# Performance work log

Hardware: AMD Instinct MI355X
Metric: run time of the kernel (lower is better)

Reference implementation:

```python
import jax, jax.numpy as jnp
import numpy as np

NUM_ACTIVE = 2  # top-k active experts

def setup_inputs() -> dict:
    key = jax.random.key(0)
    ks = jax.random.split(key, 5)
    B, N, D, H, E = 8192, 16, 128, 384, 8
    x = jax.random.normal(ks[0], (B, N, D), dtype=jnp.float32)
    # xavier-ish scales for stability
    router_w = jax.random.normal(ks[1], (E, N * D), dtype=jnp.float32) * (1.0 / np.sqrt(N * D))
    w1 = jax.random.normal(ks[2], (E, N, D, H), dtype=jnp.float32) * (1.0 / np.sqrt(D))
    w_gate = jax.random.normal(ks[3], (E, N, D, H), dtype=jnp.float32) * (1.0 / np.sqrt(D))
    w2 = jax.random.normal(ks[4], (E, N, H, D), dtype=jnp.float32) * (1.0 / np.sqrt(H))
    return {"x": x, "router_w": router_w, "w1": w1, "w_gate": w_gate, "w2": w2}

def reference(x, router_w, w1, w_gate, w2):
    B, N, D = x.shape
    E = w1.shape[0]
    # shared router over flattened heads
    router_logits = x.reshape(B, N * D) @ router_w.T            # (B, E)
    topk_logits, topk_idx = jax.lax.top_k(router_logits, NUM_ACTIVE)
    topk_w = jax.nn.softmax(topk_logits, axis=-1)               # (B, K)
    # combined routing weight per (token, expert); zero if expert not selected
    onehot = jax.nn.one_hot(topk_idx, E, dtype=x.dtype)         # (B, K, E)
    w_tok_exp = jnp.einsum('bk,bke->be', topk_w, onehot)        # (B, E)
    out = jnp.zeros_like(x)
    # loop over fixed, small expert count; unselected tokens get weight 0
    for e in range(E):
        h1 = jnp.einsum('bnd,ndh->bnh', x, w1[e])
        gate = jnp.einsum('bnd,ndh->bnh', x, w_gate[e])
        h = h1 * jax.nn.silu(gate)                              # SwiGLU (dropout=0 / eval)
        out_e = jnp.einsum('bnh,nhd->bnd', h, w2[e])
        out = out + w_tok_exp[:, e][:, None, None] * out_e
    return out
```

## Files before the change

kernel.cpp:

```cpp
#include <hip/hip_runtime.h>

#define NTOK  8192
#define NHEAD 16
#define DDIM  128
#define HDIM  384
#define NEXP  8
#define TILE  128
#define ENTRIES 1280

typedef __attribute__((ext_vector_type(8))) short short8;
typedef __attribute__((ext_vector_type(4))) float f32x4;

#define SZ_WP    (128UL*12*24*512*2)
#define OFF_WP   0UL
#define OFF_ROUT (OFF_WP + SZ_WP)
#define OFF_CNT  (OFF_ROUT + 8192UL*16)
#define OFF_TAB  (OFF_CNT + 256)
#define OFF_LIST (OFF_TAB + 2UL*ENTRIES*16)
#define OFF_WL   (OFF_LIST + 2UL*8192*4)

struct Routing { int i0, i1; float w0, w1; };

__device__ __forceinline__ unsigned short f2bf(float f) {
  unsigned int u = __float_as_uint(f);
  u += 0x7fffu + ((u >> 16) & 1u);
  return (unsigned short)(u >> 16);
}

__device__ __forceinline__ void dma16(const unsigned short* g, char* l) {
  __builtin_amdgcn_global_load_lds(
      (const __attribute__((address_space(1))) unsigned int*)g,
      (__attribute__((address_space(3))) unsigned int*)l, 16, 0, 0);
}

__global__ __launch_bounds__(256) void convA_kernel(
    const float* __restrict__ w1, const float* __restrict__ wg,
    unsigned short* __restrict__ wP) {
  __shared__ float ls[32][388];
  const int kk = blockIdx.x;
  const int en = blockIdx.y;
  const int z  = blockIdx.z;
  const float* src = (z == 0 ? w1 : wg) + ((size_t)en * DDIM + kk * 32) * HDIM;
  const int tid = threadIdx.x;
  #pragma unroll
  for (int i = 0; i < 12; ++i) {
    int f4 = i * 256 + tid;
    int row = f4 / 96, c4 = f4 % 96;
    float4 v = reinterpret_cast<const float4*>(src + (size_t)row * HDIM)[c4];
    ls[row][c4*4+0] = v.x; ls[row][c4*4+1] = v.y;
    ls[row][c4*4+2] = v.z; ls[row][c4*4+3] = v.w;
  }
  __syncthreads();
  #pragma unroll
  for (int i = 0; i < 6; ++i) {
    int fid = i * 256 + tid;
    int ct = fid >> 6, lane = fid & 63;
    int r0 = (lane >> 4) * 8, c = ct * 16 + (lane & 15);
    unsigned short o[8];
    #pragma unroll
    for (int j = 0; j < 8; ++j) o[j] = f2bf(ls[r0 + j][c]);
    size_t off = (((size_t)en * 12 + (ct >> 1)) * 24 + (z * 8 + kk * 2 + (ct & 1))) * 512
               + (size_t)lane * 8;
    reinterpret_cast<uint4*>(wP + off)[0] =
        make_uint4((unsigned)o[0] | ((unsigned)o[1] << 16),
                   (unsigned)o[2] | ((unsigned)o[3] << 16),
                   (unsigned)o[4] | ((unsigned)o[5] << 16),
                   (unsigned)o[6] | ((unsigned)o[7] << 16));
  }
}

__global__ __launch_bounds__(256) void convB_kernel(
    const float* __restrict__ w2, unsigned short* __restrict__ wP) {
  __shared__ float ls[32][132];
  const int kk = blockIdx.x;
  const int en = blockIdx.y;
  const float* src = w2 + ((size_t)en * HDIM + kk * 32) * DDIM;
  const int tid = threadIdx.x;
  #pragma unroll
  for (int i = 0; i < 4; ++i) {
    int f4 = i * 256 + tid;
    int row = f4 >> 5, c4 = f4 & 31;
    float4 v = reinterpret_cast<const float4*>(src + (size_t)row * DDIM)[c4];
    ls[row][c4*4+0] = v.x; ls[row][c4*4+1] = v.y;
    ls[row][c4*4+2] = v.z; ls[row][c4*4+3] = v.w;
  }
  __syncthreads();
  #pragma unroll
  for (int i = 0; i < 2; ++i) {
    int fid = i * 256 + tid;
    int ct = fid >> 6, lane = fid & 63;
    int r0 = (lane >> 4) * 8, c = ct * 16 + (lane & 15);
    unsigned short o[8];
    #pragma unroll
    for (int j = 0; j < 8; ++j) o[j] = f2bf(ls[r0 + j][c]);
    size_t off = (((size_t)en * 12 + kk) * 24 + (16 + ct)) * 512 + (size_t)lane * 8;
    reinterpret_cast<uint4*>(wP + off)[0] =
        make_uint4((unsigned)o[0] | ((unsigned)o[1] << 16),
                   (unsigned)o[2] | ((unsigned)o[3] << 16),
                   (unsigned)o[4] | ((unsigned)o[5] << 16),
                   (unsigned)o[6] | ((unsigned)o[7] << 16));
  }
}

__global__ __launch_bounds__(256) void router_kernel(
    const float* __restrict__ x, const float* __restrict__ rw,
    Routing* __restrict__ routing) {
  const int lane = threadIdx.x & 63;
  const int wgid = blockIdx.x * 4 + (threadIdx.x >> 6);
  const int tok0 = wgid * 4;
  float acc[4][8];
  #pragma unroll
  for (int t = 0; t < 4; ++t)
    #pragma unroll
    for (int e = 0; e < 8; ++e) acc[t][e] = 0.f;
  const float4* xr = reinterpret_cast<const float4*>(x);
  const float4* wr = reinterpret_cast<const float4*>(rw);
  #pragma unroll
  for (int c = 0; c < 8; ++c) {
    float4 wv[8];
    #pragma unroll
    for (int e = 0; e < 8; ++e) wv[e] = wr[e * 512 + c * 64 + lane];
    #pragma unroll
    for (int t = 0; t < 4; ++t) {
      float4 xv = xr[(size_t)(tok0 + t) * 512 + c * 64 + lane];
      #pragma unroll
      for (int e = 0; e < 8; ++e)
        acc[t][e] += xv.x * wv[e].x + xv.y * wv[e].y + xv.z * wv[e].z + xv.w * wv[e].w;
    }
  }
  #pragma unroll
  for (int t = 0; t < 4; ++t)
    #pragma unroll
    for (int e = 0; e < 8; ++e) {
      acc[t][e] += __shfl_xor(acc[t][e], 1);
      acc[t][e] += __shfl_xor(acc[t][e], 2);
      acc[t][e] += __shfl_xor(acc[t][e], 4);
    }
  const int l3 = lane & 7;
  #pragma unroll
  for (int t = 0; t < 4; ++t) {
    float v0 = (l3 & 1) ? acc[t][1] : acc[t][0];
    float v1 = (l3 & 1) ? acc[t][3] : acc[t][2];
    float v2 = (l3 & 1) ? acc[t][5] : acc[t][4];
    float v3 = (l3 & 1) ? acc[t][7] : acc[t][6];
    float u0 = (l3 & 2) ? v1 : v0;
    float u1 = (l3 & 2) ? v3 : v2;
    float sel = (l3 & 4) ? u1 : u0;
    sel += __shfl_xor(sel, 8);
    sel += __shfl_xor(sel, 16);
    sel += __shfl_xor(sel, 32);
    float le[8];
    #pragma unroll
    for (int e = 0; e < 8; ++e) le[e] = __shfl(sel, e);
    if (lane == 0) {
      int tok = tok0 + t;
      int i0 = 0; float m0 = le[0];
      #pragma unroll
      for (int e = 1; e < 8; ++e) if (le[e] > m0) { m0 = le[e]; i0 = e; }
      int i1 = -1; float m1 = -3.4e38f;
      #pragma unroll
      for (int e = 0; e < 8; ++e) if (e != i0 && le[e] > m1) { m1 = le[e]; i1 = e; }
      float ed = __expf(m1 - m0);
      Routing r; r.i0 = i0; r.i1 = i1;
      r.w0 = 1.f / (1.f + ed); r.w1 = ed / (1.f + ed);
      routing[tok] = r;
    }
  }
}

__global__ __launch_bounds__(256) void count_kernel(
    const Routing* __restrict__ routing, int* __restrict__ cnt) {
  const int s = blockIdx.x >> 3, e = blockIdx.x & 7;
  const int tid = threadIdx.x;
  int c = 0;
  for (int t = tid; t < NTOK; t += 256) {
    Routing r = routing[t];
    c += ((s == 0 ? r.i0 : r.i1) == e);
  }
  c += __shfl_xor(c, 32); c += __shfl_xor(c, 16); c += __shfl_xor(c, 8);
  c += __shfl_xor(c, 4);  c += __shfl_xor(c, 2);  c += __shfl_xor(c, 1);
  __shared__ int wsum[4];
  if ((tid & 63) == 0) wsum[tid >> 6] = c;
  __syncthreads();
  if (tid == 0) cnt[blockIdx.x] = wsum[0] + wsum[1] + wsum[2] + wsum[3];
}

__global__ void build_kernel(const int* __restrict__ cnt, int* __restrict__ cur,
                             int4* __restrict__ table) {
  const int tid = threadIdx.x;
  for (int i = tid; i < 2 * ENTRIES; i += 256)
    table[i] = make_int4(0, 0, 0, 0);
  __syncthreads();
  if (tid < 16) {
    int s = tid >> 3, e = tid & 7;
    int base = 0;
    for (int k = 0; k < e; ++k) base += cnt[s * 8 + k];
    cur[tid] = base;
  }
  __syncthreads();
  if (tid < 16) {
    int s = tid >> 3, xcd = tid & 7;
    int j = 0;
    int base = 0;
    for (int e = 0; e < 8; ++e) {
      int c = cnt[s * 8 + e];
      #pragma unroll
      for (int nn = 0; nn < 2; ++nn) {
        int n = xcd + nn * 8;
        for (int t = 0; t < c; t += TILE) {
          int rc = c - t; if (rc > TILE) rc = TILE;
          table[s * ENTRIES + xcd + 8 * j] = make_int4(e, base + t, rc, n);
          ++j;
        }
      }
      base += c;
    }
  }
}

__global__ __launch_bounds__(256) void compact_kernel(
    const Routing* __restrict__ routing, const int* __restrict__ cur,
    int* __restrict__ list, float* __restrict__ wl) {
  const int s = blockIdx.x >> 3, e = blockIdx.x & 7;
  const int tid = threadIdx.x;
  __shared__ int ps[256];
  int myc = 0;
  for (int t = tid; t < NTOK; t += 256) {
    Routing r = routing[t];
    myc += ((s == 0 ? r.i0 : r.i1) == e);
  }
  ps[tid] = myc;
  __syncthreads();
  for (int off = 1; off < 256; off <<= 1) {
    int v = (tid >= off) ? ps[tid - off] : 0;
    __syncthreads();
    ps[tid] += v;
    __syncthreads();
  }
  int base = cur[blockIdx.x] + ps[tid] - myc;
  for (int t = tid; t < NTOK; t += 256) {
    Routing r = routing[t];
    int ei = (s == 0 ? r.i0 : r.i1);
    if (ei == e) {
      list[s * NTOK + base] = t;
      wl[s * NTOK + base] = (s == 0 ? r.w0 : r.w1);
      ++base;
    }
  }
}

__global__ __launch_bounds__(512, 4) void expert_kernel(
    const float* __restrict__ x,
    const unsigned short* __restrict__ wP,
    const int* __restrict__ list, const float* __restrict__ wl,
    const int4* __restrict__ table,
    float* __restrict__ out, const int slot)
{
  extern __shared__ char smem[];
  char* wb  = smem;
  char* pwb = smem + 49152;
  const int4 tb = table[slot * ENTRIES + blockIdx.x];
  const int e = tb.x, rbeg = tb.y, rcnt = tb.z, n = tb.w;
  if (rcnt == 0) return;
  const int* lst = list + slot * NTOK + rbeg;
  const float* wls = wl + slot * NTOK + rbeg;
  const int tid = threadIdx.x;
  const int wid = tid >> 6, lane = tid & 63;
  const int lr = lane & 15, lq = lane >> 4;
  const int tq = wid >> 1, ch = wid & 1;
  char* pq = pwb + tq * 2304;
  const f32x4 z4 = {0.f, 0.f, 0.f, 0.f};

  const unsigned short* wsrc = wP + (size_t)(e * NHEAD + n) * (12 * 24 * 512);

  short8 a[2][4];
  #pragma unroll
  for (int mi = 0; mi < 2; ++mi) {
    int row = tq * 32 + mi * 16 + lr;
    int ok = (row < rcnt);
    int tok = ok ? lst[row] : 0;
    const float* xp = x + ((size_t)tok * NHEAD + n) * DDIM;
    #pragma unroll
    for (int kk = 0; kk < 4; ++kk) {
      const float4* q = reinterpret_cast<const float4*>(xp + kk * 32 + lq * 8);
      float4 v0 = q[0], v1 = q[1];
      if (!ok) { v0 = make_float4(0,0,0,0); v1 = make_float4(0,0,0,0); }
      short8 t;
      t[0] = (short)f2bf(v0.x); t[1] = (short)f2bf(v0.y);
      t[2] = (short)f2bf(v0.z); t[3] = (short)f2bf(v0.w);
      t[4] = (short)f2bf(v1.x); t[5] = (short)f2bf(v1.y);
      t[6] = (short)f2bf(v1.z); t[7] = (short)f2bf(v1.w);
      a[mi][kk] = t;
    }
  }

  f32x4 acc[2][4];
  #pragma unroll
  for (int mi = 0; mi < 2; ++mi)
    #pragma unroll
    for (int ct = 0; ct < 4; ++ct) acc[mi][ct] = z4;

  #pragma unroll
  for (int i = 0; i < 3; ++i) {
    int seg = wid * 3 + i;
    dma16(wsrc + (size_t)seg * 512 + lane * 8, wb + seg * 1024);
  }

  #pragma unroll
  for (int c = 0; c < 12; ++c) {
    const int p = c & 1;
    char* wbp = wb + p * 24576;

    asm volatile("s_waitcnt lgkmcnt(0)" ::: "memory");
    __builtin_amdgcn_s_barrier();
    __builtin_amdgcn_sched_barrier(0);

    if (c < 11) {
      char* wbn = wb + (p ^ 1) * 24576;
      #pragma unroll
      for (int i = 0; i < 3; ++i) {
        int seg = wid * 3 + i;
        dma16(wsrc + ((size_t)(c + 1) * 24 + seg) * 512 + lane * 8, wbn + seg * 1024);
      }
      asm volatile("s_waitcnt vmcnt(3)" ::: "memory");
    } else {
      asm volatile("s_waitcnt vmcnt(0)" ::: "memory");
    }
    __builtin_amdgcn_s_barrier();
    __builtin_amdgcn_sched_barrier(0);

    {
      f32x4 ah[2], ag[2];
      ah[0] = ah[1] = z4; ag[0] = ag[1] = z4;
      #pragma unroll
      for (int kk = 0; kk < 4; ++kk) {
        short8 b1 = *reinterpret_cast<const short8*>(wbp + (kk * 2 + ch) * 1024 + lane * 16);
        short8 bg = *reinterpret_cast<const short8*>(wbp + 8192 + (kk * 2 + ch) * 1024 + lane * 16);
        #pragma unroll
        for (int mi = 0; mi < 2; ++mi) {
          ah[mi] = __builtin_amdgcn_mfma_f32_16x16x32_bf16(a[mi][kk], b1, ah[mi], 0, 0, 0);
          ag[mi] = __builtin_amdgcn_mfma_f32_16x16x32_bf16(a[mi][kk], bg, ag[mi], 0, 0, 0);
        }
      }
      #pragma unroll
      for (int mi = 0; mi < 2; ++mi)
        #pragma unroll
        for (int r = 0; r < 4; ++r) {
          float h1 = ah[mi][r], g = ag[mi][r];
          float val = h1 * g * __builtin_amdgcn_rcpf(1.f + __expf(-g));
          int rowq = mi * 16 + lq * 4 + r;
          int h = ch * 16 + lr;
          *reinterpret_cast<unsigned short*>(pq + rowq * 72 + h * 2) = f2bf(val);
        }
    }

    asm volatile("s_waitcnt lgkmcnt(0)" ::: "memory");
    __builtin_amdgcn_s_barrier();
    __builtin_amdgcn_sched_barrier(0);

    {
      short8 a2[2];
      #pragma unroll
      for (int mi = 0; mi < 2; ++mi)
        a2[mi] = *reinterpret_cast<const short8*>(pq + (mi * 16 + lr) * 72 + lq * 16);
      #pragma unroll
      for (int ct = 0; ct < 4; ++ct) {
        short8 b = *reinterpret_cast<const short8*>(wbp + (16 + ch * 4 + ct) * 1024 + lane * 16);
        acc[0][ct] = __builtin_amdgcn_mfma_f32_16x16x32_bf16(a2[0], b, acc[0][ct], 0, 0, 0);
        acc[1][ct] = __builtin_amdgcn_mfma_f32_16x16x32_bf16(a2[1], b, acc[1][ct], 0, 0, 0);
      }
    }
  }

  #pragma unroll
  for (int mi = 0; mi < 2; ++mi)
    #pragma unroll
    for (int r = 0; r < 4; ++r) {
      int row = tq * 32 + mi * 16 + lq * 4 + r;
      if (row < rcnt) {
        int tok = lst[row];
        float wt = wls[row];
        float* op = out + ((size_t)tok * NHEAD + n) * DDIM;
        #pragma unroll
        for (int ct = 0; ct < 4; ++ct) {
          int col = (ch * 4 + ct) * 16 + lr;
          float v = acc[mi][ct][r] * wt;
          if (slot == 0) op[col] = v;
          else          op[col] += v;
        }
      }
    }
}

extern "C" void kernel_launch(void* const* d_in, const int* in_sizes, int n_in,
                              void* d_out, int out_size, void* d_ws, size_t ws_size,
                              hipStream_t stream) {
  const float* x  = (const float*)d_in[0];
  const float* rw = (const float*)d_in[1];
  const float* w1 = (const float*)d_in[2];
  const float* wg = (const float*)d_in[3];
  const float* w2 = (const float*)d_in[4];
  float* out = (float*)d_out;
  char* ws = (char*)d_ws;

  unsigned short* wP = (unsigned short*)(ws + OFF_WP);
  Routing* routing = (Routing*)(ws + OFF_ROUT);
  int* cnt = (int*)(ws + OFF_CNT);
  int* cur = cnt + 16;
  int4* table = (int4*)(ws + OFF_TAB);
  int* list = (int*)(ws + OFF_LIST);
  float* wl = (float*)(ws + OFF_WL);

  convA_kernel<<<dim3(4, 128, 2), 256, 0, stream>>>(w1, wg, wP);
  convB_kernel<<<dim3(12, 128, 1), 256, 0, stream>>>(w2, wP);
  router_kernel<<<512, 256, 0, stream>>>(x, rw, routing);
  count_kernel<<<16, 256, 0, stream>>>(routing, cnt);
  build_kernel<<<1, 256, 0, stream>>>(cnt, cur, table);
  compact_kernel<<<16, 256, 0, stream>>>(routing, cur, list, wl);
  expert_kernel<<<ENTRIES, 512, 58368, stream>>>(
      x, wP, list, wl, table, out, 0);
  expert_kernel<<<ENTRIES, 512, 58368, stream>>>(
      x, wP, list, wl, table, out, 1);
}
```

Measured before the change: 274.0 us.

## Group tokens by expert pair and fuse both expert passes into one kernel

```diff
diff --git a/kernel.cpp b/kernel.cpp
--- a/kernel.cpp
+++ b/kernel.cpp
@@ -6,7 +6,8 @@
 #define HDIM  384
 #define NEXP  8
 #define TILE  128
-#define ENTRIES 1280
+#define NPAIR 64
+#define ENTRIES 2176
 
 typedef __attribute__((ext_vector_type(8))) short short8;
 typedef __attribute__((ext_vector_type(4))) float f32x4;
@@ -15,9 +16,10 @@
 #define OFF_WP   0UL
 #define OFF_ROUT (OFF_WP + SZ_WP)
 #define OFF_CNT  (OFF_ROUT + 8192UL*16)
-#define OFF_TAB  (OFF_CNT + 256)
-#define OFF_LIST (OFF_TAB + 2UL*ENTRIES*16)
-#define OFF_WL   (OFF_LIST + 2UL*8192*4)
+#define OFF_TAB  (OFF_CNT + 512)
+#define OFF_LIST (OFF_TAB + (size_t)ENTRIES*16)
+#define OFF_WL0  (OFF_LIST + 8192UL*4)
+#define OFF_WL1  (OFF_WL0 + 8192UL*4)
 
 struct Routing { int i0, i1; float w0, w1; };
 
@@ -170,46 +172,44 @@
 
 __global__ __launch_bounds__(256) void count_kernel(
     const Routing* __restrict__ routing, int* __restrict__ cnt) {
-  const int s = blockIdx.x >> 3, e = blockIdx.x & 7;
+  const int p = blockIdx.x;
   const int tid = threadIdx.x;
   int c = 0;
   for (int t = tid; t < NTOK; t += 256) {
     Routing r = routing[t];
-    c += ((s == 0 ? r.i0 : r.i1) == e);
+    c += ((r.i0 * 8 + r.i1) == p);
   }
   c += __shfl_xor(c, 32); c += __shfl_xor(c, 16); c += __shfl_xor(c, 8);
   c += __shfl_xor(c, 4);  c += __shfl_xor(c, 2);  c += __shfl_xor(c, 1);
   __shared__ int wsum[4];
   if ((tid & 63) == 0) wsum[tid >> 6] = c;
   __syncthreads();
-  if (tid == 0) cnt[blockIdx.x] = wsum[0] + wsum[1] + wsum[2] + wsum[3];
+  if (tid == 0) cnt[p] = wsum[0] + wsum[1] + wsum[2] + wsum[3];
 }
 
 __global__ void build_kernel(const int* __restrict__ cnt, int* __restrict__ cur,
                              int4* __restrict__ table) {
   const int tid = threadIdx.x;
-  for (int i = tid; i < 2 * ENTRIES; i += 256)
+  for (int i = tid; i < ENTRIES; i += 256)
     table[i] = make_int4(0, 0, 0, 0);
   __syncthreads();
-  if (tid < 16) {
-    int s = tid >> 3, e = tid & 7;
-    int base = 0;
-    for (int k = 0; k < e; ++k) base += cnt[s * 8 + k];
-    cur[tid] = base;
-  }
-  __syncthreads();
-  if (tid < 16) {
-    int s = tid >> 3, xcd = tid & 7;
-    int j = 0;
-    int base = 0;
-    for (int e = 0; e < 8; ++e) {
-      int c = cnt[s * 8 + e];
+  if (tid < NPAIR) {
+    int b = 0;
+    for (int k = 0; k < tid; ++k) b += cnt[k];
+    cur[tid] = b;
+  }
+  __syncthreads();
+  if (tid < 8) {
+    int xcd = tid;
+    int j = 0, base = 0;
+    for (int p = 0; p < NPAIR; ++p) {
+      int c = cnt[p];
       #pragma unroll
       for (int nn = 0; nn < 2; ++nn) {
         int n = xcd + nn * 8;
         for (int t = 0; t < c; t += TILE) {
           int rc = c - t; if (rc > TILE) rc = TILE;
-          table[s * ENTRIES + xcd + 8 * j] = make_int4(e, base + t, rc, n);
+          table[xcd + 8 * j] = make_int4(p, base + t, rc, n);
           ++j;
         }
       }
@@ -220,14 +220,14 @@
 
 __global__ __launch_bounds__(256) void compact_kernel(
     const Routing* __restrict__ routing, const int* __restrict__ cur,
-    int* __restrict__ list, float* __restrict__ wl) {
-  const int s = blockIdx.x >> 3, e = blockIdx.x & 7;
+    int* __restrict__ list, float* __restrict__ wl0, float* __restrict__ wl1) {
+  const int p = blockIdx.x;
   const int tid = threadIdx.x;
   __shared__ int ps[256];
   int myc = 0;
   for (int t = tid; t < NTOK; t += 256) {
     Routing r = routing[t];
-    myc += ((s == 0 ? r.i0 : r.i1) == e);
+    myc += ((r.i0 * 8 + r.i1) == p);
   }
   ps[tid] = myc;
   __syncthreads();
@@ -237,33 +237,36 @@
     ps[tid] += v;
     __syncthreads();
   }
-  int base = cur[blockIdx.x] + ps[tid] - myc;
+  int base = cur[p] + ps[tid] - myc;
   for (int t = tid; t < NTOK; t += 256) {
     Routing r = routing[t];
-    int ei = (s == 0 ? r.i0 : r.i1);
-    if (ei == e) {
-      list[s * NTOK + base] = t;
-      wl[s * NTOK + base] = (s == 0 ? r.w0 : r.w1);
+    if ((r.i0 * 8 + r.i1) == p) {
+      list[base] = t;
+      wl0[base] = r.w0;
+      wl1[base] = r.w1;
       ++base;
     }
   }
 }
 
-__global__ __launch_bounds__(512, 4) void expert_kernel(
+__global__ __launch_bounds__(512, 3) void expert_kernel(
     const float* __restrict__ x,
     const unsigned short* __restrict__ wP,
-    const int* __restrict__ list, const float* __restrict__ wl,
+    const int* __restrict__ list,
+    const float* __restrict__ wl0, const float* __restrict__ wl1,
     const int4* __restrict__ table,
-    float* __restrict__ out, const int slot)
+    float* __restrict__ out)
 {
   extern __shared__ char smem[];
   char* wb  = smem;
   char* pwb = smem + 49152;
-  const int4 tb = table[slot * ENTRIES + blockIdx.x];
-  const int e = tb.x, rbeg = tb.y, rcnt = tb.z, n = tb.w;
+  const int4 tb = table[blockIdx.x];
+  const int pair = tb.x, rbeg = tb.y, rcnt = tb.z, n = tb.w;
   if (rcnt == 0) return;
-  const int* lst = list + slot * NTOK + rbeg;
-  const float* wls = wl + slot * NTOK + rbeg;
+  const int e0 = pair >> 3, e1 = pair & 7;
+  const int* lst = list + rbeg;
+  const float* wls0 = wl0 + rbeg;
+  const float* wls1 = wl1 + rbeg;
   const int tid = threadIdx.x;
   const int wid = tid >> 6, lane = tid & 63;
   const int lr = lane & 15, lq = lane >> 4;
@@ -271,7 +274,8 @@
   char* pq = pwb + tq * 2304;
   const f32x4 z4 = {0.f, 0.f, 0.f, 0.f};
 
-  const unsigned short* wsrc = wP + (size_t)(e * NHEAD + n) * (12 * 24 * 512);
+  const unsigned short* wsrc0 = wP + (size_t)(e0 * NHEAD + n) * (12 * 24 * 512);
+  const unsigned short* wsrc1 = wP + (size_t)(e1 * NHEAD + n) * (12 * 24 * 512);
 
   short8 a[2][4];
   #pragma unroll
@@ -294,33 +298,37 @@
     }
   }
 
-  f32x4 acc[2][4];
+  f32x4 acc0[2][4], acc1[2][4];
   #pragma unroll
   for (int mi = 0; mi < 2; ++mi)
     #pragma unroll
-    for (int ct = 0; ct < 4; ++ct) acc[mi][ct] = z4;
+    for (int ct = 0; ct < 4; ++ct) { acc0[mi][ct] = z4; acc1[mi][ct] = z4; }
 
   #pragma unroll
   for (int i = 0; i < 3; ++i) {
     int seg = wid * 3 + i;
-    dma16(wsrc + (size_t)seg * 512 + lane * 8, wb + seg * 1024);
-  }
-
-  #pragma unroll
-  for (int c = 0; c < 12; ++c) {
-    const int p = c & 1;
+    dma16(wsrc0 + (size_t)seg * 512 + lane * 8, wb + seg * 1024);
+  }
+
+  #pragma unroll
+  for (int g = 0; g < 24; ++g) {
+    const int p = g & 1;
     char* wbp = wb + p * 24576;
 
     asm volatile("s_waitcnt lgkmcnt(0)" ::: "memory");
     __builtin_amdgcn_s_barrier();
     __builtin_amdgcn_sched_barrier(0);
 
-    if (c < 11) {
+    if (g < 23) {
+      const int gn = g + 1;
+      const unsigned short* nsrc = (gn < 12)
+          ? wsrc0 + (size_t)gn * (24 * 512)
+          : wsrc1 + (size_t)(gn - 12) * (24 * 512);
       char* wbn = wb + (p ^ 1) * 24576;
       #pragma unroll
       for (int i = 0; i < 3; ++i) {
         int seg = wid * 3 + i;
-        dma16(wsrc + ((size_t)(c + 1) * 24 + seg) * 512 + lane * 8, wbn + seg * 1024);
+        dma16(nsrc + (size_t)seg * 512 + lane * 8, wbn + seg * 1024);
       }
       asm volatile("s_waitcnt vmcnt(3)" ::: "memory");
     } else {
@@ -346,8 +354,8 @@
       for (int mi = 0; mi < 2; ++mi)
         #pragma unroll
         for (int r = 0; r < 4; ++r) {
-          float h1 = ah[mi][r], g = ag[mi][r];
-          float val = h1 * g * __builtin_amdgcn_rcpf(1.f + __expf(-g));
+          float h1 = ah[mi][r], gg = ag[mi][r];
+          float val = h1 * gg * __builtin_amdgcn_rcpf(1.f + __expf(-gg));
           int rowq = mi * 16 + lq * 4 + r;
           int h = ch * 16 + lr;
           *reinterpret_cast<unsigned short*>(pq + rowq * 72 + h * 2) = f2bf(val);
@@ -359,6 +367,7 @@
     __builtin_amdgcn_sched_barrier(0);
 
     {
+      auto& acc = (g < 12) ? acc0 : acc1;
       short8 a2[2];
       #pragma unroll
       for (int mi = 0; mi < 2; ++mi)
@@ -379,14 +388,12 @@
       int row = tq * 32 + mi * 16 + lq * 4 + r;
       if (row < rcnt) {
         int tok = lst[row];
-        float wt = wls[row];
+        float wt0 = wls0[row], wt1 = wls1[row];
         float* op = out + ((size_t)tok * NHEAD + n) * DDIM;
         #pragma unroll
         for (int ct = 0; ct < 4; ++ct) {
           int col = (ch * 4 + ct) * 16 + lr;
-          float v = acc[mi][ct][r] * wt;
-          if (slot == 0) op[col] = v;
-          else          op[col] += v;
+          op[col] = acc0[mi][ct][r] * wt0 + acc1[mi][ct][r] * wt1;
         }
       }
     }
@@ -406,19 +413,18 @@
   unsigned short* wP = (unsigned short*)(ws + OFF_WP);
   Routing* routing = (Routing*)(ws + OFF_ROUT);
   int* cnt = (int*)(ws + OFF_CNT);
-  int* cur = cnt + 16;
+  int* cur = cnt + NPAIR;
   int4* table = (int4*)(ws + OFF_TAB);
   int* list = (int*)(ws + OFF_LIST);
-  float* wl = (float*)(ws + OFF_WL);
+  float* wl0 = (float*)(ws + OFF_WL0);
+  float* wl1 = (float*)(ws + OFF_WL1);
 
   convA_kernel<<<dim3(4, 128, 2), 256, 0, stream>>>(w1, wg, wP);
   convB_kernel<<<dim3(12, 128, 1), 256, 0, stream>>>(w2, wP);
   router_kernel<<<512, 256, 0, stream>>>(x, rw, routing);
-  count_kernel<<<16, 256, 0, stream>>>(routing, cnt);
+  count_kernel<<<NPAIR, 256, 0, stream>>>(routing, cnt);
   build_kernel<<<1, 256, 0, stream>>>(cnt, cur, table);
-  compact_kernel<<<16, 256, 0, stream>>>(routing, cur, list, wl);
+  compact_kernel<<<NPAIR, 256, 0, stream>>>(routing, cur, list, wl0, wl1);
   expert_kernel<<<ENTRIES, 512, 58368, stream>>>(
-      x, wP, list, wl, table, out, 0);
-  expert_kernel<<<ENTRIES, 512, 58368, stream>>>(
-      x, wP, list, wl, table, out, 1);
-}
+      x, wP, list, wl0, wl1, table, out);
+}
```

After: 355.3 us. +29.7%, slower.
